# Performance work log

Measured on AMD Instinct MI355X. Metric: run time of the kernel, lower is better.

Reference implementation:

```python
import jax, jax.numpy as jnp
import numpy as np

N_NODES, E_TOT, E_ACT = 20000, 250000, 200000
LAT, OH = 128, 128
M0, M1, M2 = 64, 32, 16            # irreps_out: 64x0e + 32x1o + 16x2e
D_IR = M0 + 3 * M1 + 5 * M2        # 240
G = M1 + M2                        # gate scalars (48)
T0 = M0 + G                        # tp m=0 scalar channels (112)
I0, I1, I2 = 3 * M0, 3 * M1, 3 * M2  # tp input muls (center|edge|neighbor)


def _split(x, m0, m1, m2):
    e = x.shape[0]
    return (x[:, :m0],
            x[:, m0:m0 + 3 * m1].reshape(e, m1, 3),
            x[:, m0 + 3 * m1:].reshape(e, m2, 5))


def _merge(s0, s1, s2):
    e = s0.shape[0]
    return jnp.concatenate([s0, s1.reshape(e, -1), s2.reshape(e, -1)], axis=-1)


def _mlp(x, ws, bs):
    for i, (w, b) in enumerate(zip(ws, bs)):
        x = x @ w + b
        if i < len(ws) - 1:
            x = jax.nn.silu(x)
    return x


def _forward(latents, node_features, edge_features, cutoff_coeffs, edge_one_hot,
             wigner_D1, wigner_D2,
             W0, W1r, W1i, W2r, W2i, Gw, Gb,
             P0, P0b, P1, P2, Ew, Eb, ln_g, ln_b,
             A1, A1b, A2, A2b, A3, A3b,
             B1, B1b, B2, B2b, B3, B3b,
             O0, O1, O2,
             edge_index, active_edges):
    ec = edge_index[0][active_edges]
    en = edge_index[1][active_edges]
    # gather node features per edge (equivariant_norm_type='none' -> identity norms)
    nc0, nc1, nc2 = _split(node_features[ec], M0, M1, M2)
    ef0, ef1, ef2 = _split(edge_features, M0, M1, M2)
    nn0, nn1, nn2 = _split(node_features[en], M0, M1, M2)
    x0 = jnp.concatenate([nc0, ef0, nn0], -1)   # [E,192]
    x1 = jnp.concatenate([nc1, ef1, nn1], 1)    # [E,96,3]
    x2 = jnp.concatenate([nc2, ef2, nn2], 1)    # [E,48,5]
    lat_a = latents[active_edges]
    # --- SO(2) linear: rotate into edge frame, per-m mixing, latent gains, rotate back ---
    r1 = jnp.einsum('eij,euj->eui', wigner_D1, x1)
    r2 = jnp.einsum('eij,euj->eui', wigner_D2, x2)
    in0 = jnp.concatenate([x0, r1[:, :, 1], r2[:, :, 2]], -1)   # m=0 [E,336]
    o_m0 = in0 @ W0.T                                           # [E,160]
    ip1 = jnp.concatenate([r1[:, :, 2], r2[:, :, 3]], -1)       # m=+1 [E,144]
    im1 = jnp.concatenate([r1[:, :, 0], r2[:, :, 1]], -1)       # m=-1
    op1 = ip1 @ W1r.T - im1 @ W1i.T                             # [E,48]
    on1 = ip1 @ W1i.T + im1 @ W1r.T
    op2 = r2[:, :, 4] @ W2r.T - r2[:, :, 0] @ W2i.T             # [E,16]
    on2 = r2[:, :, 4] @ W2i.T + r2[:, :, 0] @ W2r.T
    g = lat_a @ Gw + Gb                                         # per-edge gains [E,224]
    o_m0 = o_m0 * g[:, :160]
    g1 = g[:, 160:208]; g2 = g[:, 208:224]
    op1 = op1 * g1; on1 = on1 * g1; op2 = op2 * g2; on2 = on2 * g2
    y0 = o_m0[:, :T0]
    y1 = jnp.stack([on1[:, :M1], o_m0[:, T0:T0 + M1], op1[:, :M1]], -1)          # [E,32,3]
    y2 = jnp.stack([on2, on1[:, M1:], o_m0[:, T0 + M1:], op1[:, M1:], op2], -1)  # [E,16,5]
    y1 = jnp.einsum('eji,euj->eui', wigner_D1, y1)
    y2 = jnp.einsum('eji,euj->eui', wigner_D2, y2)
    # --- gate activation ---
    gates = jax.nn.sigmoid(y0[:, M0:])
    z0 = jax.nn.silu(y0[:, :M0])
    z1 = y1 * gates[:, :M1, None]
    z2 = y2 * gates[:, M1:, None]
    # --- lin_post: per-l channel mixing, fan-in normalized, bias on scalars ---
    z0 = z0 @ P0.T / np.sqrt(M0) + P0b
    z1 = jnp.einsum('uv,evm->eum', P1, z1) / np.sqrt(M1)
    z2 = jnp.einsum('uv,evm->eum', P2, z2) / np.sqrt(M2)
    scalars = z0                                               # taken before weighting
    # --- E3ElementLinear: per-edge per-channel weights from latents ---
    w = lat_a @ Ew + Eb                                        # [E,112]
    z0 = z0 * w[:, :M0]
    z1 = z1 * w[:, M0:M0 + M1, None]
    z2 = z2 * w[:, M0 + M1:, None]
    new_edge = _merge(z0, z1, z2)
    # --- latent update: LN -> mlp1(ln_lat||scalars) -> mlp2(h||one_hot) -> cutoff ---
    mu = lat_a.mean(-1, keepdims=True)
    var = ((lat_a - mu) ** 2).mean(-1, keepdims=True)
    ln_lat = (lat_a - mu) * jax.lax.rsqrt(var + 1e-5) * ln_g + ln_b
    h = _mlp(jnp.concatenate([ln_lat, scalars], -1), (A1, A2, A3), (A1b, A2b, A3b))
    h = _mlp(jnp.concatenate([h, edge_one_hot], -1), (B1, B2, B3), (B1b, B2b, B3b))
    new_lat = cutoff_coeffs[active_edges][:, None] * h
    # --- residual update (res_update_params buffer = 0) ---
    u = jax.nn.sigmoid(jnp.asarray(0.0, new_edge.dtype))
    c_old = jax.lax.rsqrt(u * u + 1.0)
    c_new = u * c_old
    edge_out = c_old * edge_features + c_new * new_edge        # identity residual path
    latents_out = latents.at[active_edges].set(c_new * new_lat + c_old * lat_a)
    # --- layer one-hot tensor product (uvu with 128x0e) ---
    f0, f1, f2 = _split(edge_out, M0, M1, M2)
    s = 1.0 / np.sqrt(OH)
    t0 = f0 * (edge_one_hot @ O0.T) * s
    t1 = f1 * (edge_one_hot @ O1.T)[:, :, None] * s
    t2 = f2 * (edge_one_hot @ O2.T)[:, :, None] * s
    edge_out = edge_out + _merge(t0, t1, t2)
    return edge_out, latents_out


def setup_inputs() -> dict:
    key = jax.random.key(0)
    ks = iter(jax.random.split(key, 64))
    nrm = lambda sh, s=0.05: jax.random.normal(next(ks), sh, jnp.float32) * s
    inp = dict(
        latents=nrm((E_TOT, LAT), 1.0),
        node_features=nrm((N_NODES, D_IR), 1.0),
        edge_features=nrm((E_ACT, D_IR), 1.0),
        cutoff_coeffs=jax.random.uniform(next(ks), (E_TOT,), jnp.float32),
        edge_one_hot=jax.random.uniform(next(ks), (E_ACT, OH), jnp.float32),
        wigner_D1=nrm((E_ACT, 3, 3), 0.5),
        wigner_D2=nrm((E_ACT, 5, 5), 0.3),
        W0=nrm((160, I0 + I1 + I2)), W1r=nrm((48, 144)), W1i=nrm((48, 144)),
        W2r=nrm((16, 48)), W2i=nrm((16, 48)),
        Gw=nrm((LAT, 224)), Gb=jnp.ones((224,), jnp.float32),
        P0=nrm((M0, M0)), P0b=nrm((M0,)), P1=nrm((M1, M1)), P2=nrm((M2, M2)),
        Ew=nrm((LAT, M0 + M1 + M2)), Eb=jnp.ones((M0 + M1 + M2,), jnp.float32),
        ln_g=jnp.ones((LAT,), jnp.float32), ln_b=jnp.zeros((LAT,), jnp.float32),
        A1=nrm((LAT + M0, LAT)), A1b=nrm((LAT,)),
        A2=nrm((LAT, LAT)), A2b=nrm((LAT,)),
        A3=nrm((LAT, LAT)), A3b=nrm((LAT,)),
        B1=nrm((LAT + OH, LAT)), B1b=nrm((LAT,)),
        B2=nrm((LAT, LAT)), B2b=nrm((LAT,)),
        B3=nrm((LAT, LAT)), B3b=nrm((LAT,)),
        O0=nrm((M0, OH)), O1=nrm((M1, OH)), O2=nrm((M2, OH)),
        edge_index=jax.random.randint(next(ks), (2, E_TOT), 0, N_NODES, jnp.int32),
        active_edges=jnp.sort(jax.random.permutation(next(ks), E_TOT)[:E_ACT]).astype(jnp.int32),
    )
    return inp


def reference(latents, node_features, edge_features, cutoff_coeffs, edge_one_hot,
              wigner_D1, wigner_D2,
              W0, W1r, W1i, W2r, W2i, Gw, Gb,
              P0, P0b, P1, P2, Ew, Eb, ln_g, ln_b,
              A1, A1b, A2, A2b, A3, A3b,
              B1, B1b, B2, B2b, B3, B3b,
              O0, O1, O2, edge_index, active_edges):
    return _forward(latents, node_features, edge_features, cutoff_coeffs, edge_one_hot,
                    wigner_D1, wigner_D2,
                    W0, W1r, W1i, W2r, W2i, Gw, Gb,
                    P0, P0b, P1, P2, Ew, Eb, ln_g, ln_b,
                    A1, A1b, A2, A2b, A3, A3b,
                    B1, B1b, B2, B2b, B3, B3b,
                    O0, O1, O2, edge_index, active_edges)
```

## Files before the change

### kernel.cpp

```cpp
#include <hip/hip_runtime.h>

typedef unsigned short us_t;
typedef short bf16x8 __attribute__((ext_vector_type(8)));
typedef float f32x4 __attribute__((ext_vector_type(4)));

#define E_ACT 200000
#define E_TOT 250000
#define DIR   240
#define C_OLD 0.8944271909999159f
#define C_NEW 0.4472135954999579f
#define S_OH  0.08838834764831845f

#define WO_W0   0
#define WO_W1P  56320
#define WO_W1M  70144
#define WO_W2P  83968
#define WO_W2M  85504
#define WO_GW   87040
#define WO_EW   115712
#define WO_A1   130048
#define WO_A2   154624
#define WO_A3   171008
#define WO_B1   187392
#define WO_B2   220160
// ... 102 lines not shown
        a[ks] = av;
    }
}

__device__ __forceinline__ void gemmW0g(
    const us_t* __restrict__ in0s, const us_t* __restrict__ wbase,
    const bf16x8 latA[4], const float* __restrict__ Gb,
    int nt0, int nt1, us_t* __restrict__ om0g, int lane)
{
    const int r = lane & 15, g = lane >> 4;
    f32x4 w0a = {0.f,0.f,0.f,0.f}, w0b = w0a, ga = w0a, gb2 = w0a;
    const us_t* ap  = in0s + r * 360 + g * 8;
    const us_t* wp0 = wbase + WO_W0 + (size_t)(nt0 * 16 + r) * 352 + g * 8;
    const us_t* wp1 = wbase + WO_W0 + (size_t)(nt1 * 16 + r) * 352 + g * 8;
    #pragma unroll
    for (int ks = 0; ks < 11; ++ks) {
        bf16x8 a = *(const bf16x8*)(ap + ks * 32);
        w0a = MFMA(a, *(const bf16x8*)(wp0 + ks * 32), w0a);
        w0b = MFMA(a, *(const bf16x8*)(wp1 + ks * 32), w0b);
    }
    const us_t* gp0 = wbase + WO_GW + (size_t)(nt0 * 16 + r) * 128 + g * 8;
    const us_t* gp1 = wbase + WO_GW + (size_t)(nt1 * 16 + r) * 128 + g * 8;
    #pragma unroll
    for (int ks = 0; ks < 4; ++ks) {
        ga  = MFMA(latA[ks], *(const bf16x8*)(gp0 + ks * 32), ga);
        gb2 = MFMA(latA[ks], *(const bf16x8*)(gp1 + ks * 32), gb2);
    }
    float b0 = Gb[nt0 * 16 + r], b1 = Gb[nt1 * 16 + r];
    #pragma unroll
    for (int i = 0; i < 4; ++i) {
        int e = g * 4 + i;
        om0g[e * 162 + nt0 * 16 + r] = f2b(w0a[i] * (ga[i] + b0));
        om0g[e * 162 + nt1 * 16 + r] = f2b(w0b[i] * (gb2[i] + b1));
    }
}

__device__ __forceinline__ void gemmW1g(
    const us_t* __restrict__ cact1, const us_t* __restrict__ wbase,
    const bf16x8 latA[4], const float* __restrict__ Gb,
    int j, us_t* __restrict__ cp1g, us_t* __restrict__ cn1g, int lane)
{
    const int r = lane & 15, g = lane >> 4;
    f32x4 p = {0.f,0.f,0.f,0.f}, m = p, gg = p;
    const us_t* ap  = cact1 + r * 296 + g * 8;
    const us_t* wpP = wbase + WO_W1P + (size_t)(j * 16 + r) * 288 + g * 8;
    const us_t* wpM = wbase + WO_W1M + (size_t)(j * 16 + r) * 288 + g * 8;
    #pragma unroll
    for (int ks = 0; ks < 9; ++ks) {
        bf16x8 a = *(const bf16x8*)(ap + ks * 32);
        p = MFMA(a, *(const bf16x8*)(wpP + ks * 32), p);
        m = MFMA(a, *(const bf16x8*)(wpM + ks * 32), m);
    }
    const us_t* gp = wbase + WO_GW + (size_t)(160 + j * 16 + r) * 128 + g * 8;
    #pragma unroll
    for (int ks = 0; ks < 4; ++ks)
        gg = MFMA(latA[ks], *(const bf16x8*)(gp + ks * 32), gg);
    float gb = Gb[160 + j * 16 + r];
    #pragma unroll
    for (int i = 0; i < 4; ++i) {
        int e = g * 4 + i;
        float gv = gg[i] + gb;
        cp1g[e * 50 + j * 16 + r] = f2b(p[i] * gv);
        cn1g[e * 50 + j * 16 + r] = f2b(m[i] * gv);
    }
}

__device__ __forceinline__ void gemmW2g(
    const us_t* __restrict__ cact2, const us_t* __restrict__ wbase,
    const bf16x8 latA[4], const float* __restrict__ Gb,
    us_t* __restrict__ cp2g, us_t* __restrict__ cn2g, int lane)
{
    const int r = lane & 15, g = lane >> 4;
    f32x4 p = {0.f,0.f,0.f,0.f}, m = p, gg = p;
    const us_t* ap  = cact2 + r * 104 + g * 8;
    const us_t* wpP = wbase + WO_W2P + (size_t)r * 96 + g * 8;
    const us_t* wpM = wbase + WO_W2M + (size_t)r * 96 + g * 8;
    #pragma unroll
    for (int ks = 0; ks < 3; ++ks) {
        bf16x8 a = *(const bf16x8*)(ap + ks * 32);
        p = MFMA(a, *(const bf16x8*)(wpP + ks * 32), p);
        m = MFMA(a, *(const bf16x8*)(wpM + ks * 32), m);
    }
    const us_t* gp = wbase + WO_GW + (size_t)(208 + r) * 128 + g * 8;
    #pragma unroll
    for (int ks = 0; ks < 4; ++ks)
        gg = MFMA(latA[ks], *(const bf16x8*)(gp + ks * 32), gg);
    float gb = Gb[208 + r];
    #pragma unroll
    for (int i = 0; i < 4; ++i) {
        int e = g * 4 + i;
        float gv = gg[i] + gb;
        cp2g[e * 18 + r] = f2b(p[i] * gv);
        cn2g[e * 18 + r] = f2b(m[i] * gv);
    }
}

__device__ __forceinline__ void lat_gemm2(const bf16x8 a[4],
    const us_t* __restrict__ wgt, const float* __restrict__ bias,
    int nt0, int nt1, us_t* __restrict__ out, int os, int lane)
{
    const int r = lane & 15, g = lane >> 4;
    f32x4 acc0 = {0.f,0.f,0.f,0.f}, acc1 = {0.f,0.f,0.f,0.f};
    const us_t* wp0 = wgt + (size_t)(nt0 * 16 + r) * 128 + g * 8;
    const us_t* wp1 = wgt + (size_t)(nt1 * 16 + r) * 128 + g * 8;
    #pragma unroll
    for (int ks = 0; ks < 4; ++ks) {
        acc0 = MFMA(a[ks], *(const bf16x8*)(wp0 + ks * 32), acc0);
        acc1 = MFMA(a[ks], *(const bf16x8*)(wp1 + ks * 32), acc1);
    }
    float bi0 = bias[nt0 * 16 + r], bi1 = bias[nt1 * 16 + r];
    #pragma unroll
    for (int i = 0; i < 4; ++i) {
        int e = g * 4 + i;
        out[e * os + nt0 * 16 + r] = f2b(acc0[i] + bi0);
        out[e * os + nt1 * 16 + r] = f2b(acc1[i] + bi1);
    }
}

__device__ __forceinline__ void lat_gemm1(const bf16x8 a[4],
    const us_t* __restrict__ wgt, const float* __restrict__ bias,
    int nt, us_t* __restrict__ out, int os, int lane)
{
    const int r = lane & 15, g = lane >> 4;
    f32x4 acc = {0.f,0.f,0.f,0.f};
    const us_t* wp = wgt + (size_t)(nt * 16 + r) * 128 + g * 8;
    #pragma unroll
    for (int ks = 0; ks < 4; ++ks)
        acc = MFMA(a[ks], *(const bf16x8*)(wp + ks * 32), acc);
    float bi = bias[nt * 16 + r];
    #pragma unroll
    for (int i = 0; i < 4; ++i) {
        int e = g * 4 + i;
        out[e * os + nt * 16 + r] = f2b(acc[i] + bi);
    }
}

template<int KS>
__device__ __forceinline__ f32x4 pgemm(const us_t* __restrict__ actbase, int as,
                                       const us_t* __restrict__ wgt, int kp, int lane)
{
    const int r = lane & 15, g = lane >> 4;
    f32x4 acc = {0.f,0.f,0.f,0.f};
    const us_t* ap = actbase + r * as + g * 8;
    const us_t* wp = wgt + (size_t)r * kp + g * 8;
    #pragma unroll
    for (int ks = 0; ks < KS; ++ks) {
        bf16x8 a = *(const bf16x8*)(ap + ks * 32);
        bf16x8 b = *(const bf16x8*)(wp + ks * 32);
        acc = MFMA(a, b, acc);
    }
    return acc;
}

__global__ __launch_bounds__(256, 3) void k1_kernel(
    const float* __restrict__ latents,
    const float* __restrict__ node_features,
    const float* __restrict__ edge_features,
    const float* __restrict__ wD1,
    const float* __restrict__ wD2,
    const float* __restrict__ Gb,  const float* __restrict__ Eb,
    const float* __restrict__ P0b,
    const int* __restrict__ edge_index, const int* __restrict__ active_edges,
    const us_t* __restrict__ wbase,
    us_t* __restrict__ ne_ws, us_t* __restrict__ scal_ws)
{
    __shared__ __align__(16) char smem[40320];
    us_t* in0s  = (us_t*)(smem);
    us_t* cact1 = (us_t*)(smem + 11520);
    us_t* cact2 = (us_t*)(smem + 20992);
    float* D1l  = (float*)(smem + 24320);
    float* D2l  = (float*)(smem + 25088);
    int*   aes  = (int*)(smem + 26880);
    us_t* om0g  = (us_t*)(smem + 26944);
    us_t* cp1g  = (us_t*)(smem + 32128);
    us_t* cn1g  = (us_t*)(smem + 33728);
    us_t* cp2g  = (us_t*)(smem + 35328);
    us_t* cn2g  = (us_t*)(smem + 35904);
    us_t* wl    = (us_t*)(smem + 36480);
    us_t* z0l   = (us_t*)(smem);
    us_t* z1l   = (us_t*)(smem + 2304);
    us_t* z2l   = (us_t*)(smem + 5632);

    const int t  = threadIdx.x;
    const int e0 = blockIdx.x * 16;

    {
        const int e = t >> 4, l = t & 15;
        const int eg = e0 + e;
        const int ae = active_edges[eg];
        const int ec = edge_index[ae];
        const int en = edge_index[E_TOT + ae];
        if (l == 0) aes[e] = ae;

        float v1  = (l < 9) ? wD1[(size_t)eg * 9 + l] : 0.f;
        float v2a = wD2[(size_t)eg * 25 + l];
        float v2b = (l < 9) ? wD2[(size_t)eg * 25 + 16 + l] : 0.f;
        if (l < 9) D1l[e * 12 + l] = v1;
        D2l[e * 28 + l] = v2a;
        if (l < 9) D2l[e * 28 + 16 + l] = v2b;

        float d1[9], d2[25];
        #pragma unroll
        for (int i = 0; i < 9; ++i)  d1[i] = __shfl(v1, i, 16);
        #pragma unroll
        for (int i = 0; i < 16; ++i) d2[i] = __shfl(v2a, i, 16);
        #pragma unroll
        for (int i = 0; i < 9; ++i)  d2[16 + i] = __shfl(v2b, i, 16);

        const float* pc = node_features + (size_t)ec * DIR;
        const float* pe = edge_features + (size_t)eg * DIR;
        const float* pn = node_features + (size_t)en * DIR;
        us_t* in0 = in0s + e * 360;
        us_t* c1  = cact1 + e * 296;
        us_t* c2  = cact2 + e * 104;

        #pragma unroll
        for (int j = 0; j < 4; ++j) {
            int i = l + 16 * j;
            in0[i]       = f2b(pc[i]);
            in0[64 + i]  = f2b(pe[i]);
            in0[128 + i] = f2b(pn[i]);
        }
        in0[336 + l] = 0;

        #pragma unroll
        for (int jj = 0; jj < 6; ++jj) {
            int u = l + 16 * jj;
            int uu = u & 31;
            const float* sp = (u < 32 ? pc : (u < 64 ? pe : pn)) + 64 + uu * 3;
            float x0 = sp[0], x1 = sp[1], x2 = sp[2];
            float r0 = d1[0] * x0 + d1[1] * x1 + d1[2] * x2;
            float r1 = d1[3] * x0 + d1[4] * x1 + d1[5] * x2;
            float r2 = d1[6] * x0 + d1[7] * x1 + d1[8] * x2;
            c1[144 + u]  = f2b(r0);
            in0[192 + u] = f2b(r1);
            c1[u]        = f2b(r2);
        }
        #pragma unroll
        for (int jj = 0; jj < 3; ++jj) {
            int u = l + 16 * jj;
            int uu = u & 15;
            const float* sp = (u < 16 ? pc : (u < 32 ? pe : pn)) + 160 + uu * 5;
            float x0 = sp[0], x1 = sp[1], x2 = sp[2], x3 = sp[3], x4 = sp[4];
            float r[5];
            #pragma unroll
            for (int i = 0; i < 5; ++i)
                r[i] = d2[i * 5 + 0] * x0 + d2[i * 5 + 1] * x1 + d2[i * 5 + 2] * x2
                     + d2[i * 5 + 3] * x3 + d2[i * 5 + 4] * x4;
            c2[48 + u]   = f2b(r[0]);
            c1[240 + u]  = f2b(r[1]);
            in0[288 + u] = f2b(r[2]);
            c1[96 + u]   = f2b(r[3]);
            c2[u]        = f2b(r[4]);
        }
    }
    __syncthreads();

    {
        const int lane = t & 63, w = t >> 6;
        bf16x8 a[4];
        lat_fetch_a(latents, aes, lane, a);
        if (w == 0) {
            gemmW0g(in0s, wbase, a, Gb, 0, 1, om0g, lane);
            gemmW0g(in0s, wbase, a, Gb, 2, 3, om0g, lane);
        } else if (w == 1) {
            gemmW0g(in0s, wbase, a, Gb, 4, 5, om0g, lane);
            gemmW0g(in0s, wbase, a, Gb, 6, 7, om0g, lane);
        } else if (w == 2) {
            gemmW1g(cact1, wbase, a, Gb, 0, cp1g, cn1g, lane);
            gemmW1g(cact1, wbase, a, Gb, 1, cp1g, cn1g, lane);
            gemmW1g(cact1, wbase, a, Gb, 2, cp1g, cn1g, lane);
        } else {
            gemmW0g(in0s, wbase, a, Gb, 8, 9, om0g, lane);
            gemmW2g(cact2, wbase, a, Gb, cp2g, cn2g, lane);
            lat_gemm2(a, wbase + WO_EW, Eb, 0, 1, wl, 120, lane);
            lat_gemm2(a, wbase + WO_EW, Eb, 2, 3, wl, 120, lane);
            lat_gemm2(a, wbase + WO_EW, Eb, 4, 5, wl, 120, lane);
            lat_gemm1(a, wbase + WO_EW, Eb, 6, wl, 120, lane);
        }
    }
    __syncthreads();

    {
        const int e = t >> 4, l = t & 15;
        const float* D1e = D1l + e * 12;
        const float* D2e = D2l + e * 28;
        #pragma unroll
        for (int uu = 0; uu < 2; ++uu) {
            int u = l + uu * 16;
            float j0 = b2f(cn1g[e * 50 + u]);
            float j1 = b2f(om0g[e * 162 + 112 + u]);
            float j2 = b2f(cp1g[e * 50 + u]);
            float gate = sigm(b2f(om0g[e * 162 + 64 + u]));
            #pragma unroll
            for (int i = 0; i < 3; ++i) {
                float yr = D1e[0 * 3 + i] * j0 + D1e[1 * 3 + i] * j1 + D1e[2 * 3 + i] * j2;
                z1l[e * 104 + i * 32 + u] = f2b(yr * gate);
            }
        }
        {
            int u = l;
            float j0 = b2f(cn2g[e * 18 + u]);
            float j1 = b2f(cn1g[e * 50 + 32 + u]);
            float j2 = b2f(om0g[e * 162 + 144 + u]);
            float j3 = b2f(cp1g[e * 50 + 32 + u]);
            float j4 = b2f(cp2g[e * 18 + u]);
            float gate = sigm(b2f(om0g[e * 162 + 96 + u]));
            #pragma unroll
            for (int i = 0; i < 5; ++i) {
                float yr = D2e[0 * 5 + i] * j0 + D2e[1 * 5 + i] * j1 + D2e[2 * 5 + i] * j2
                         + D2e[3 * 5 + i] * j3 + D2e[4 * 5 + i] * j4;
                z2l[e * 168 + i * 32 + u] = f2b(yr * gate);
                z2l[e * 168 + i * 32 + 16 + u] = 0;
            }
        }
        #pragma unroll
        for (int ii = 0; ii < 4; ++ii) {
            int c = l + 16 * ii;
            float v = b2f(om0g[e * 162 + c]);
            z0l[e * 72 + c] = f2b(v * sigm(v));
        }
    }
    __syncthreads();

    {
        const int lane = t & 63, w = t >> 6;
        const int r = lane & 15, g = lane >> 4;
        if (w < 2) {
            #pragma unroll
            for (int jj = 0; jj < 2; ++jj) {
                int nt = 2 * w + jj;
                f32x4 acc = pgemm<2>(z0l, 72, wbase + WO_P0T + nt * 16 * 64, 64, lane);
                int n = nt * 16 + r;
                float bi = P0b[n];
                #pragma unroll
                for (int i = 0; i < 4; ++i) {
                    int e = g * 4 + i, eg = e0 + e;
                    float z0p = acc[i] * 0.125f + bi;
                    scal_ws[(size_t)eg * 64 + n] = f2b(z0p);
                    ne_ws[(size_t)eg * 240 + n] = f2b(z0p * b2f(wl[e * 120 + n]));
                }
            }
        } else if (w == 2) {
            #pragma unroll
            for (int m = 0; m < 3; ++m) {
                #pragma unroll
                for (int nt = 0; nt < 2; ++nt) {
                    f32x4 acc = pgemm<1>(z1l + m * 32, 104,
                                         wbase + WO_P1T + nt * 16 * 32, 32, lane);
                    int u = nt * 16 + r;
                    #pragma unroll
                    for (int i = 0; i < 4; ++i) {
                        int e = g * 4 + i, eg = e0 + e;
                        float wv = b2f(wl[e * 120 + 64 + u]);
                        ne_ws[(size_t)eg * 240 + 64 + u * 3 + m] =
                            f2b(acc[i] * 0.17677669529663687f * wv);
                    }
                }
            }
        } else if (w == 3) {
            #pragma unroll
            for (int m = 0; m < 5; ++m) {
                f32x4 acc = pgemm<1>(z2l + m * 32, 168, wbase + WO_P2T, 32, lane);
                int u = r;
                #pragma unroll
                for (int i = 0; i < 4; ++i) {
                    int e = g * 4 + i, eg = e0 + e;
                    float wv = b2f(wl[e * 120 + 96 + u]);
                    ne_ws[(size_t)eg * 240 + 160 + u * 5 + m] =
                        f2b(acc[i] * 0.25f * wv);
                }
            }
        }
    }
}

template<int KS, bool SILU>
__device__ __forceinline__ void mlayer(
    const us_t* __restrict__ actA, const us_t* __restrict__ actB, int split, int as,
    const us_t* __restrict__ wgt, int kp, const float* __restrict__ bias,
    us_t* __restrict__ out, int os, int lane, int w)
{
    const int r = lane & 15, g = lane >> 4;
    const int n0 = 2 * w * 16, n1 = n0 + 16;
    f32x4 a00 = {0.f,0.f,0.f,0.f}, a01 = a00, a10 = a00, a11 = a00;
    const us_t* wp0 = wgt + (size_t)(n0 + r) * kp + g * 8;
    const us_t* wp1 = wgt + (size_t)(n1 + r) * kp + g * 8;
    #pragma unroll
    for (int ks = 0; ks < KS; ++ks) {
        const us_t* ab = (ks < split) ? (actA + ks * 32) : (actB + (ks - split) * 32);
        bf16x8 f0 = *(const bf16x8*)(ab + r * as + g * 8);
        bf16x8 f1 = *(const bf16x8*)(ab + (16 + r) * as + g * 8);
        bf16x8 b0 = *(const bf16x8*)(wp0 + ks * 32);
        bf16x8 b1 = *(const bf16x8*)(wp1 + ks * 32);
        a00 = MFMA(f0, b0, a00); a01 = MFMA(f0, b1, a01);
        a10 = MFMA(f1, b0, a10); a11 = MFMA(f1, b1, a11);
    }
    float bi0 = bias[n0 + r], bi1 = bias[n1 + r];
    #pragma unroll
    for (int i = 0; i < 4; ++i) {
        int eA = g * 4 + i, eB = 16 + g * 4 + i;
        float v;
        v = a00[i] + bi0; if (SILU) v *= sigm(v); out[eA * os + n0 + r] = f2b(v);
        v = a01[i] + bi1; if (SILU) v *= sigm(v); out[eA * os + n1 + r] = f2b(v);
        v = a10[i] + bi0; if (SILU) v *= sigm(v); out[eB * os + n0 + r] = f2b(v);
        v = a11[i] + bi1; if (SILU) v *= sigm(v); out[eB * os + n1 + r] = f2b(v);
    }
}

__global__ __launch_bounds__(256) void k2_kernel(
    const float* __restrict__ latents, const float* __restrict__ cutoff,
    const float* __restrict__ one_hot,
    const float* __restrict__ ln_g, const float* __restrict__ ln_b,
    const float* __restrict__ A1b, const float* __restrict__ A2b, const float* __restrict__ A3b,
    const float* __restrict__ B1b, const float* __restrict__ B2b, const float* __restrict__ B3b,
    const int* __restrict__ active_edges,
    const us_t* __restrict__ wbase,
    const us_t* __restrict__ scal_ws, us_t* __restrict__ ohw_ws,
    float* __restrict__ out_lat)
{
    __shared__ __align__(16) char smem[39424];
    us_t* x_lds = (us_t*)(smem);
    us_t* h_a   = (us_t*)(smem + 12800);
    us_t* h_b   = (us_t*)(smem + 21504);
    us_t* ohl   = (us_t*)(smem + 30208);
    int*  aes_l = (int*)(smem + 38912);
    float* cut_l= (float*)(smem + 39040);

    const int t  = threadIdx.x;
    const int e0 = blockIdx.x * 32;
    const int lane = t & 63, w = t >> 6;

    {
        int ee = t >> 3, l8 = t & 7;
        int ae = active_edges[e0 + ee];
        if (l8 == 0) { aes_l[ee] = ae; cut_l[ee] = cutoff[ae]; }
        const float* lp = latents + (size_t)ae * 128 + l8 * 16;
        float xs[16];
        #pragma unroll
        for (int q = 0; q < 4; ++q) {
            float4 v = *(const float4*)(lp + q * 4);
            xs[q * 4 + 0] = v.x; xs[q * 4 + 1] = v.y;
            xs[q * 4 + 2] = v.z; xs[q * 4 + 3] = v.w;
        }
        float s1 = 0.f, s2 = 0.f;
        #pragma unroll
        for (int i = 0; i < 16; ++i) { s1 += xs[i]; s2 += xs[i] * xs[i]; }
        #pragma unroll
        for (int off = 1; off < 8; off <<= 1) {
            s1 += __shfl_xor(s1, off, 8);
            s2 += __shfl_xor(s2, off, 8);
        }
        float mu  = s1 * (1.f / 128.f);
        float var = s2 * (1.f / 128.f) - mu * mu;
        float rstd = rsqrtf(var + 1e-5f);
        #pragma unroll
        for (int i = 0; i < 16; ++i) {
            int li = l8 * 16 + i;
            x_lds[ee * 200 + li] = f2b((xs[i] - mu) * rstd * ln_g[li] + ln_b[li]);
        }
    }
    for (int idx = t; idx < 32 * 16; idx += 256) {
        int ee = idx >> 4, j = idx & 15;
        *(ushort4*)&x_lds[ee * 200 + 128 + j * 4] =
            *(const ushort4*)&scal_ws[(size_t)(e0 + ee) * 64 + j * 4];
    }
    for (int idx = t; idx < 32 * 32; idx += 256) {
        int ee = idx >> 5, j = idx & 31;
        float4 ov = *(const float4*)&one_hot[(size_t)(e0 + ee) * 128 + j * 4];
        ushort4 s; s.x = f2b(ov.x); s.y = f2b(ov.y); s.z = f2b(ov.z); s.w = f2b(ov.w);
        *(ushort4*)&ohl[ee * 136 + j * 4] = s;
    }
    __syncthreads();

    mlayer<6, true>(x_lds, x_lds, 6, 200, wbase + WO_A1, 192, A1b, h_a, 136, lane, w);
    __syncthreads();
    mlayer<4, true>(h_a, h_a, 4, 136, wbase + WO_A2, 128, A2b, h_b, 136, lane, w);
    __syncthreads();
    mlayer<4, false>(h_b, h_b, 4, 136, wbase + WO_A3, 128, A3b, h_a, 136, lane, w);
    __syncthreads();
    mlayer<8, true>(h_a, ohl, 4, 136, wbase + WO_B1, 256, B1b, h_b, 136, lane, w);
    __syncthreads();
    mlayer<4, true>(h_b, h_b, 4, 136, wbase + WO_B2, 128, B2b, h_a, 136, lane, w);
    __syncthreads();
    {
        const int r = lane & 15, g = lane >> 4;
        const int n0 = 2 * w * 16, n1 = n0 + 16;
        f32x4 a00 = {0.f,0.f,0.f,0.f}, a01 = a00, a10 = a00, a11 = a00;
        const us_t* wp0 = wbase + WO_B3 + (size_t)(n0 + r) * 128 + g * 8;
        const us_t* wp1 = wbase + WO_B3 + (size_t)(n1 + r) * 128 + g * 8;
        #pragma unroll
        for (int ks = 0; ks < 4; ++ks) {
            bf16x8 f0 = *(const bf16x8*)(h_a + ks * 32 + r * 136 + g * 8);
            bf16x8 f1 = *(const bf16x8*)(h_a + ks * 32 + (16 + r) * 136 + g * 8);
            bf16x8 b0 = *(const bf16x8*)(wp0 + ks * 32);
            bf16x8 b1 = *(const bf16x8*)(wp1 + ks * 32);
            a00 = MFMA(f0, b0, a00); a01 = MFMA(f0, b1, a01);
            a10 = MFMA(f1, b0, a10); a11 = MFMA(f1, b1, a11);
        }
        float bi0 = B3b[n0 + r], bi1 = B3b[n1 + r];
        #pragma unroll
        for (int i = 0; i < 4; ++i) {
            int eA = g * 4 + i, eB = 16 + g * 4 + i;
            int aeA = aes_l[eA], aeB = aes_l[eB];
            float cA = C_NEW * cut_l[eA], cB = C_NEW * cut_l[eB];
            float* oA = out_lat + (size_t)aeA * 128;
            float* oB = out_lat + (size_t)aeB * 128;
            const float* lA = latents + (size_t)aeA * 128;
            const float* lB = latents + (size_t)aeB * 128;
            oA[n0 + r] = cA * (a00[i] + bi0) + C_OLD * lA[n0 + r];
            oA[n1 + r] = cA * (a01[i] + bi1) + C_OLD * lA[n1 + r];
            oB[n0 + r] = cB * (a10[i] + bi0) + C_OLD * lB[n0 + r];
            oB[n1 + r] = cB * (a11[i] + bi1) + C_OLD * lB[n1 + r];
        }
    }

    {
        const int r = lane & 15, g = lane >> 4;
        const int cnt = (w == 3) ? 1 : 2;
        #pragma unroll
        for (int ii = 0; ii < 2; ++ii) {
            if (ii >= cnt) break;
            int nt = (ii == 0) ? w : w + 4;
            const us_t* wb2 = (nt < 4) ? (wbase + WO_O0 + (size_t)nt * 16 * 128)
                            : (nt < 6) ? (wbase + WO_O1 + (size_t)(nt - 4) * 16 * 128)
                                       : (wbase + WO_O2);
            f32x4 c0 = {0.f,0.f,0.f,0.f}, c1 = c0;
            const us_t* wp = wb2 + (size_t)r * 128 + g * 8;
            #pragma unroll
            for (int ks = 0; ks < 4; ++ks) {
                bf16x8 f0 = *(const bf16x8*)(ohl + ks * 32 + r * 136 + g * 8);
                bf16x8 f1 = *(const bf16x8*)(ohl + ks * 32 + (16 + r) * 136 + g * 8);
                bf16x8 b = *(const bf16x8*)(wp + ks * 32);
                c0 = MFMA(f0, b, c0); c1 = MFMA(f1, b, c1);
            }
            int n = nt * 16 + r;
            #pragma unroll
            for (int i = 0; i < 4; ++i) {
                int eA = e0 + g * 4 + i, eB = e0 + 16 + g * 4 + i;
                ohw_ws[(size_t)eA * 112 + n] = f2b(c0[i]);
                ohw_ws[(size_t)eB * 112 + n] = f2b(c1[i]);
            }
        }
    }
}

__global__ __launch_bounds__(256) void kfin_kernel(
    const float* __restrict__ edge_features, const us_t* __restrict__ ne_ws,
    const us_t* __restrict__ ohw_ws, float* __restrict__ out_edge)
{
    int idx = blockIdx.x * 256 + threadIdx.x;
    if (idx >= E_ACT * 60) return;
    int e = idx / 60;
    int c0 = (idx - e * 60) * 4;
    float4 ef = *(const float4*)&edge_features[(size_t)e * 240 + c0];
    ushort4 nv = *(const ushort4*)&ne_ws[(size_t)e * 240 + c0];
    float nef[4] = {b2f(nv.x), b2f(nv.y), b2f(nv.z), b2f(nv.w)};
    float eff[4] = {ef.x, ef.y, ef.z, ef.w};
    float4 ov;
    float* op = &ov.x;
    #pragma unroll
    for (int j = 0; j < 4; ++j) {
        int c = c0 + j;
        int o;
        if (c < 64)       o = c;
        else if (c < 160) o = 64 + (c - 64) / 3;
        else              o = 96 + (c - 160) / 5;
        float ohv = b2f(ohw_ws[(size_t)e * 112 + o]);
        op[j] = (C_OLD * eff[j] + C_NEW * nef[j]) * (1.f + S_OH * ohv);
    }
    *(float4*)&out_edge[(size_t)e * 240 + c0] = ov;
}

extern "C" void kernel_launch(void* const* d_in, const int* in_sizes, int n_in,
                              void* d_out, int out_size, void* d_ws, size_t ws_size,
                              hipStream_t stream)
{
    const float* latents  = (const float*)d_in[0];
    const float* node_f   = (const float*)d_in[1];
    const float* edge_f   = (const float*)d_in[2];
    const float* cutoff   = (const float*)d_in[3];
    const float* one_hot  = (const float*)d_in[4];
    const float* wD1      = (const float*)d_in[5];
    const float* wD2      = (const float*)d_in[6];
    const float* W0       = (const float*)d_in[7];
    const float* W1r      = (const float*)d_in[8];
    const float* W1i      = (const float*)d_in[9];
    const float* W2r      = (const float*)d_in[10];
    const float* W2i      = (const float*)d_in[11];
    const float* Gw       = (const float*)d_in[12];
    const float* Gb       = (const float*)d_in[13];
    const float* P0w      = (const float*)d_in[14];
    const float* P0b      = (const float*)d_in[15];
    const float* P1w      = (const float*)d_in[16];
    const float* P2w      = (const float*)d_in[17];
    const float* Ew       = (const float*)d_in[18];
    const float* Eb       = (const float*)d_in[19];
    const float* ln_g     = (const float*)d_in[20];
    const float* ln_b     = (const float*)d_in[21];
    const float* A1       = (const float*)d_in[22];
    const float* A1b      = (const float*)d_in[23];
    const float* A2       = (const float*)d_in[24];
    const float* A2b      = (const float*)d_in[25];
    const float* A3       = (const float*)d_in[26];
    const float* A3b      = (const float*)d_in[27];
    const float* B1       = (const float*)d_in[28];
    const float* B1b      = (const float*)d_in[29];
    const float* B2       = (const float*)d_in[30];
    const float* B2b      = (const float*)d_in[31];
    const float* B3       = (const float*)d_in[32];
    const float* B3b      = (const float*)d_in[33];
    const float* O0       = (const float*)d_in[34];
    const float* O1       = (const float*)d_in[35];
    const float* O2       = (const float*)d_in[36];
    const int* edge_index = (const int*)d_in[37];
    const int* act_e      = (const int*)d_in[38];

    float* out_edge = (float*)d_out;
    float* out_lat  = out_edge + (size_t)E_ACT * DIR;

    us_t* ne_ws   = (us_t*)d_ws;
    us_t* ohw_ws  = ne_ws + (size_t)E_ACT * DIR;
    us_t* scal_ws = ohw_ws + (size_t)E_ACT * 112;
    us_t* wbase   = scal_ws + (size_t)E_ACT * 64;

    prep_kernel<<<dim3((W_TOTAL + 255) / 256), dim3(256), 0, stream>>>(
        W0, W1r, W1i, W2r, W2i, Gw, Ew, A1, A2, A3, B1, B2, B3,
        O0, O1, O2, P0w, P1w, P2w, wbase);

    hipMemcpyAsync(out_lat, latents, (size_t)E_TOT * 128 * sizeof(float),
                   hipMemcpyDeviceToDevice, stream);

    k1_kernel<<<dim3(E_ACT / 16), dim3(256), 0, stream>>>(
        latents, node_f, edge_f, wD1, wD2, Gb, Eb, P0b,
        edge_index, act_e, wbase, ne_ws, scal_ws);

    k2_kernel<<<dim3(E_ACT / 32), dim3(256), 0, stream>>>(
        latents, cutoff, one_hot, ln_g, ln_b,
        A1b, A2b, A3b, B1b, B2b, B3b,
        act_e, wbase, scal_ws, ohw_ws, out_lat);

    kfin_kernel<<<dim3((E_ACT * 60 + 255) / 256), dim3(256), 0, stream>>>(
        edge_f, ne_ws, ohw_ws, out_edge);
}
```

Before: 806.6 us.

## Double block size to 512 threads and redistribute MFMA tiles across eight waves

Both fused kernels go from 256 to 512 threads per block (8 waves) and keep the same edges per block. Each phase's work is split more finely: per-edge elementwise work uses 32 lanes per edge, the W0/W1/W2/Ew GEMMs are spread over 8 waves, and the k2 MLP layers compute one 16-column tile per wave instead of two. The aim is more parallelism per block and shorter per-wave critical paths between barriers. The cost is more waves per block and some idle lanes, and launch_bounds (512,6) may force register pressure or spills.

```diff
diff --git a/kernel.cpp b/kernel.cpp
--- a/kernel.cpp
+++ b/kernel.cpp
@@ -278,7 +278,7 @@
     return acc;
 }
 
-__global__ __launch_bounds__(256, 3) void k1_kernel(
+__global__ __launch_bounds__(512, 6) void k1_kernel(
     const float* __restrict__ latents,
     const float* __restrict__ node_features,
     const float* __restrict__ edge_features,
@@ -311,27 +311,23 @@
     const int e0 = blockIdx.x * 16;
 
     {
-        const int e = t >> 4, l = t & 15;
+        const int e = t >> 5, l = t & 31;
         const int eg = e0 + e;
         const int ae = active_edges[eg];
         const int ec = edge_index[ae];
         const int en = edge_index[E_TOT + ae];
         if (l == 0) aes[e] = ae;
 
-        float v1  = (l < 9) ? wD1[(size_t)eg * 9 + l] : 0.f;
-        float v2a = wD2[(size_t)eg * 25 + l];
-        float v2b = (l < 9) ? wD2[(size_t)eg * 25 + 16 + l] : 0.f;
-        if (l < 9) D1l[e * 12 + l] = v1;
-        D2l[e * 28 + l] = v2a;
-        if (l < 9) D2l[e * 28 + 16 + l] = v2b;
+        float v1  = (l < 9)  ? wD1[(size_t)eg * 9 + l]  : 0.f;
+        float v2a = (l < 25) ? wD2[(size_t)eg * 25 + l] : 0.f;
+        if (l < 9)  D1l[e * 12 + l] = v1;
+        if (l < 25) D2l[e * 28 + l] = v2a;
 
         float d1[9], d2[25];
         #pragma unroll
-        for (int i = 0; i < 9; ++i)  d1[i] = __shfl(v1, i, 16);
-        #pragma unroll
-        for (int i = 0; i < 16; ++i) d2[i] = __shfl(v2a, i, 16);
-        #pragma unroll
-        for (int i = 0; i < 9; ++i)  d2[16 + i] = __shfl(v2b, i, 16);
+        for (int i = 0; i < 9; ++i)  d1[i] = __shfl(v1, i, 32);
+        #pragma unroll
+        for (int i = 0; i < 25; ++i) d2[i] = __shfl(v2a, i, 32);
 
         const float* pc = node_features + (size_t)ec * DIR;
         const float* pe = edge_features + (size_t)eg * DIR;
@@ -341,17 +337,17 @@
         us_t* c2  = cact2 + e * 104;
 
         #pragma unroll
-        for (int j = 0; j < 4; ++j) {
-            int i = l + 16 * j;
+        for (int j = 0; j < 2; ++j) {
+            int i = l + 32 * j;
             in0[i]       = f2b(pc[i]);
             in0[64 + i]  = f2b(pe[i]);
             in0[128 + i] = f2b(pn[i]);
         }
-        in0[336 + l] = 0;
-
-        #pragma unroll
-        for (int jj = 0; jj < 6; ++jj) {
-            int u = l + 16 * jj;
+        if (l < 16) in0[336 + l] = 0;
+
+        #pragma unroll
+        for (int jj = 0; jj < 3; ++jj) {
+            int u = l + 32 * jj;
             int uu = u & 31;
             const float* sp = (u < 32 ? pc : (u < 64 ? pe : pn)) + 64 + uu * 3;
             float x0 = sp[0], x1 = sp[1], x2 = sp[2];
@@ -363,21 +359,23 @@
             c1[u]        = f2b(r2);
         }
         #pragma unroll
-        for (int jj = 0; jj < 3; ++jj) {
-            int u = l + 16 * jj;
-            int uu = u & 15;
-            const float* sp = (u < 16 ? pc : (u < 32 ? pe : pn)) + 160 + uu * 5;
-            float x0 = sp[0], x1 = sp[1], x2 = sp[2], x3 = sp[3], x4 = sp[4];
-            float r[5];
-            #pragma unroll
-            for (int i = 0; i < 5; ++i)
-                r[i] = d2[i * 5 + 0] * x0 + d2[i * 5 + 1] * x1 + d2[i * 5 + 2] * x2
-                     + d2[i * 5 + 3] * x3 + d2[i * 5 + 4] * x4;
-            c2[48 + u]   = f2b(r[0]);
-            c1[240 + u]  = f2b(r[1]);
-            in0[288 + u] = f2b(r[2]);
-            c1[96 + u]   = f2b(r[3]);
-            c2[u]        = f2b(r[4]);
+        for (int jj = 0; jj < 2; ++jj) {
+            int u = l + 32 * jj;
+            if (u < 48) {
+                int uu = u & 15;
+                const float* sp = (u < 16 ? pc : (u < 32 ? pe : pn)) + 160 + uu * 5;
+                float x0 = sp[0], x1 = sp[1], x2 = sp[2], x3 = sp[3], x4 = sp[4];
+                float r[5];
+                #pragma unroll
+                for (int i = 0; i < 5; ++i)
+                    r[i] = d2[i * 5 + 0] * x0 + d2[i * 5 + 1] * x1 + d2[i * 5 + 2] * x2
+                         + d2[i * 5 + 3] * x3 + d2[i * 5 + 4] * x4;
+                c2[48 + u]   = f2b(r[0]);
+                c1[240 + u]  = f2b(r[1]);
+                in0[288 + u] = f2b(r[2]);
+                c1[96 + u]   = f2b(r[3]);
+                c2[u]        = f2b(r[4]);
+            }
         }
     }
     __syncthreads();
@@ -386,19 +384,15 @@
         const int lane = t & 63, w = t >> 6;
         bf16x8 a[4];
         lat_fetch_a(latents, aes, lane, a);
-        if (w == 0) {
-            gemmW0g(in0s, wbase, a, Gb, 0, 1, om0g, lane);
-            gemmW0g(in0s, wbase, a, Gb, 2, 3, om0g, lane);
-        } else if (w == 1) {
-            gemmW0g(in0s, wbase, a, Gb, 4, 5, om0g, lane);
-            gemmW0g(in0s, wbase, a, Gb, 6, 7, om0g, lane);
-        } else if (w == 2) {
+        if (w < 5) {
+            gemmW0g(in0s, wbase, a, Gb, 2 * w, 2 * w + 1, om0g, lane);
+        } else if (w == 5) {
             gemmW1g(cact1, wbase, a, Gb, 0, cp1g, cn1g, lane);
             gemmW1g(cact1, wbase, a, Gb, 1, cp1g, cn1g, lane);
+        } else if (w == 6) {
             gemmW1g(cact1, wbase, a, Gb, 2, cp1g, cn1g, lane);
+            gemmW2g(cact2, wbase, a, Gb, cp2g, cn2g, lane);
         } else {
-            gemmW0g(in0s, wbase, a, Gb, 8, 9, om0g, lane);
-            gemmW2g(cact2, wbase, a, Gb, cp2g, cn2g, lane);
             lat_gemm2(a, wbase + WO_EW, Eb, 0, 1, wl, 120, lane);
             lat_gemm2(a, wbase + WO_EW, Eb, 2, 3, wl, 120, lane);
             lat_gemm2(a, wbase + WO_EW, Eb, 4, 5, wl, 120, lane);
@@ -408,12 +402,11 @@
     __syncthreads();
 
     {
-        const int e = t >> 4, l = t & 15;
+        const int e = t >> 5, l = t & 31;
         const float* D1e = D1l + e * 12;
         const float* D2e = D2l + e * 28;
-        #pragma unroll
-        for (int uu = 0; uu < 2; ++uu) {
-            int u = l + uu * 16;
+        {
+            int u = l;
             float j0 = b2f(cn1g[e * 50 + u]);
             float j1 = b2f(om0g[e * 162 + 112 + u]);
             float j2 = b2f(cp1g[e * 50 + u]);
@@ -424,7 +417,7 @@
                 z1l[e * 104 + i * 32 + u] = f2b(yr * gate);
             }
         }
-        {
+        if (l < 16) {
             int u = l;
             float j0 = b2f(cn2g[e * 18 + u]);
             float j1 = b2f(cn1g[e * 50 + 32 + u]);
@@ -441,8 +434,8 @@
             }
         }
         #pragma unroll
-        for (int ii = 0; ii < 4; ++ii) {
-            int c = l + 16 * ii;
+        for (int ii = 0; ii < 2; ++ii) {
+            int c = l + 32 * ii;
             float v = b2f(om0g[e * 162 + c]);
             z0l[e * 72 + c] = f2b(v * sigm(v));
         }
@@ -452,49 +445,45 @@
     {
         const int lane = t & 63, w = t >> 6;
         const int r = lane & 15, g = lane >> 4;
-        if (w < 2) {
+        const float sc1 = 0.17677669529663687f;
+        if (w < 4) {
+            f32x4 acc = pgemm<2>(z0l, 72, wbase + WO_P0T + w * 16 * 64, 64, lane);
+            int n = w * 16 + r;
+            float bi = P0b[n];
             #pragma unroll
-            for (int jj = 0; jj < 2; ++jj) {
-                int nt = 2 * w + jj;
-                f32x4 acc = pgemm<2>(z0l, 72, wbase + WO_P0T + nt * 16 * 64, 64, lane);
-                int n = nt * 16 + r;
-                float bi = P0b[n];
+            for (int i = 0; i < 4; ++i) {
+                int e = g * 4 + i, eg = e0 + e;
+                float z0p = acc[i] * 0.125f + bi;
+                scal_ws[(size_t)eg * 64 + n] = f2b(z0p);
+                ne_ws[(size_t)eg * 240 + n] = f2b(z0p * b2f(wl[e * 120 + n]));
+            }
+        } else if (w == 4 || w == 5) {
+            #pragma unroll
+            for (int q = 0; q < 3; ++q) {
+                int idx = (w - 4) * 3 + q;
+                int m = idx >> 1, nt = idx & 1;
+                f32x4 acc = pgemm<1>(z1l + m * 32, 104,
+                                     wbase + WO_P1T + nt * 16 * 32, 32, lane);
+                int u = nt * 16 + r;
                 #pragma unroll
                 for (int i = 0; i < 4; ++i) {
                     int e = g * 4 + i, eg = e0 + e;
-                    float z0p = acc[i] * 0.125f + bi;
-                    scal_ws[(size_t)eg * 64 + n] = f2b(z0p);
-                    ne_ws[(size_t)eg * 240 + n] = f2b(z0p * b2f(wl[e * 120 + n]));
+                    float wv = b2f(wl[e * 120 + 64 + u]);
+                    ne_ws[(size_t)eg * 240 + 64 + u * 3 + m] = f2b(acc[i] * sc1 * wv);
                 }
             }
-        } else if (w == 2) {
-            #pragma unroll
-            for (int m = 0; m < 3; ++m) {
-                #pragma unroll
-                for (int nt = 0; nt < 2; ++nt) {
-                    f32x4 acc = pgemm<1>(z1l + m * 32, 104,
-                                         wbase + WO_P1T + nt * 16 * 32, 32, lane);
-                    int u = nt * 16 + r;
-                    #pragma unroll
-                    for (int i = 0; i < 4; ++i) {
-                        int e = g * 4 + i, eg = e0 + e;
-                        float wv = b2f(wl[e * 120 + 64 + u]);
-                        ne_ws[(size_t)eg * 240 + 64 + u * 3 + m] =
-                            f2b(acc[i] * 0.17677669529663687f * wv);
-                    }
-                }
-            }
-        } else if (w == 3) {
-            #pragma unroll
-            for (int m = 0; m < 5; ++m) {
+        } else {
+            const int mstart = (w == 6) ? 0 : 3;
+            const int mcnt   = (w == 6) ? 3 : 2;
+            for (int q = 0; q < mcnt; ++q) {
+                int m = mstart + q;
                 f32x4 acc = pgemm<1>(z2l + m * 32, 168, wbase + WO_P2T, 32, lane);
                 int u = r;
                 #pragma unroll
                 for (int i = 0; i < 4; ++i) {
                     int e = g * 4 + i, eg = e0 + e;
                     float wv = b2f(wl[e * 120 + 96 + u]);
-                    ne_ws[(size_t)eg * 240 + 160 + u * 5 + m] =
-                        f2b(acc[i] * 0.25f * wv);
+                    ne_ws[(size_t)eg * 240 + 160 + u * 5 + m] = f2b(acc[i] * 0.25f * wv);
                 }
             }
         }
@@ -502,39 +491,35 @@
 }
 
 template<int KS, bool SILU>
-__device__ __forceinline__ void mlayer(
+__device__ __forceinline__ void mlayer8(
     const us_t* __restrict__ actA, const us_t* __restrict__ actB, int split, int as,
     const us_t* __restrict__ wgt, int kp, const float* __restrict__ bias,
     us_t* __restrict__ out, int os, int lane, int w)
 {
     const int r = lane & 15, g = lane >> 4;
-    const int n0 = 2 * w * 16, n1 = n0 + 16;
-    f32x4 a00 = {0.f,0.f,0.f,0.f}, a01 = a00, a10 = a00, a11 = a00;
-    const us_t* wp0 = wgt + (size_t)(n0 + r) * kp + g * 8;
-    const us_t* wp1 = wgt + (size_t)(n1 + r) * kp + g * 8;
+    const int n0 = w * 16;
+    f32x4 a0 = {0.f,0.f,0.f,0.f}, a1 = a0;
+    const us_t* wp = wgt + (size_t)(n0 + r) * kp + g * 8;
     #pragma unroll
     for (int ks = 0; ks < KS; ++ks) {
         const us_t* ab = (ks < split) ? (actA + ks * 32) : (actB + (ks - split) * 32);
         bf16x8 f0 = *(const bf16x8*)(ab + r * as + g * 8);
         bf16x8 f1 = *(const bf16x8*)(ab + (16 + r) * as + g * 8);
-        bf16x8 b0 = *(const bf16x8*)(wp0 + ks * 32);
-        bf16x8 b1 = *(const bf16x8*)(wp1 + ks * 32);
-        a00 = MFMA(f0, b0, a00); a01 = MFMA(f0, b1, a01);
-        a10 = MFMA(f1, b0, a10); a11 = MFMA(f1, b1, a11);
-    }
-    float bi0 = bias[n0 + r], bi1 = bias[n1 + r];
+        bf16x8 b = *(const bf16x8*)(wp + ks * 32);
+        a0 = MFMA(f0, b, a0);
+        a1 = MFMA(f1, b, a1);
+    }
+    float bi = bias[n0 + r];
     #pragma unroll
     for (int i = 0; i < 4; ++i) {
         int eA = g * 4 + i, eB = 16 + g * 4 + i;
         float v;
-        v = a00[i] + bi0; if (SILU) v *= sigm(v); out[eA * os + n0 + r] = f2b(v);
-        v = a01[i] + bi1; if (SILU) v *= sigm(v); out[eA * os + n1 + r] = f2b(v);
-        v = a10[i] + bi0; if (SILU) v *= sigm(v); out[eB * os + n0 + r] = f2b(v);
-        v = a11[i] + bi1; if (SILU) v *= sigm(v); out[eB * os + n1 + r] = f2b(v);
-    }
-}
-
-__global__ __launch_bounds__(256) void k2_kernel(
+        v = a0[i] + bi; if (SILU) v *= sigm(v); out[eA * os + n0 + r] = f2b(v);
+        v = a1[i] + bi; if (SILU) v *= sigm(v); out[eB * os + n0 + r] = f2b(v);
+    }
+}
+
+__global__ __launch_bounds__(512, 6) void k2_kernel(
     const float* __restrict__ latents, const float* __restrict__ cutoff,
     const float* __restrict__ one_hot,
     const float* __restrict__ ln_g, const float* __restrict__ ln_b,
@@ -558,40 +543,36 @@
     const int lane = t & 63, w = t >> 6;
 
     {
-        int ee = t >> 3, l8 = t & 7;
+        int ee = t >> 4, l16 = t & 15;
         int ae = active_edges[e0 + ee];
-        if (l8 == 0) { aes_l[ee] = ae; cut_l[ee] = cutoff[ae]; }
-        const float* lp = latents + (size_t)ae * 128 + l8 * 16;
-        float xs[16];
-        #pragma unroll
-        for (int q = 0; q < 4; ++q) {
-            float4 v = *(const float4*)(lp + q * 4);
-            xs[q * 4 + 0] = v.x; xs[q * 4 + 1] = v.y;
-            xs[q * 4 + 2] = v.z; xs[q * 4 + 3] = v.w;
-        }
+        if (l16 == 0) { aes_l[ee] = ae; cut_l[ee] = cutoff[ae]; }
+        const float* lp = latents + (size_t)ae * 128 + l16 * 8;
+        float4 va = *(const float4*)lp;
+        float4 vb = *(const float4*)(lp + 4);
+        float xs[8] = {va.x, va.y, va.z, va.w, vb.x, vb.y, vb.z, vb.w};
         float s1 = 0.f, s2 = 0.f;
         #pragma unroll
-        for (int i = 0; i < 16; ++i) { s1 += xs[i]; s2 += xs[i] * xs[i]; }
-        #pragma unroll
-        for (int off = 1; off < 8; off <<= 1) {
-            s1 += __shfl_xor(s1, off, 8);
-            s2 += __shfl_xor(s2, off, 8);
+        for (int i = 0; i < 8; ++i) { s1 += xs[i]; s2 += xs[i] * xs[i]; }
+        #pragma unroll
+        for (int off = 1; off < 16; off <<= 1) {
+            s1 += __shfl_xor(s1, off, 16);
+            s2 += __shfl_xor(s2, off, 16);
         }
         float mu  = s1 * (1.f / 128.f);
         float var = s2 * (1.f / 128.f) - mu * mu;
         float rstd = rsqrtf(var + 1e-5f);
         #pragma unroll
-        for (int i = 0; i < 16; ++i) {
-            int li = l8 * 16 + i;
+        for (int i = 0; i < 8; ++i) {
+            int li = l16 * 8 + i;
             x_lds[ee * 200 + li] = f2b((xs[i] - mu) * rstd * ln_g[li] + ln_b[li]);
         }
     }
-    for (int idx = t; idx < 32 * 16; idx += 256) {
+    for (int idx = t; idx < 32 * 16; idx += 512) {
         int ee = idx >> 4, j = idx & 15;
         *(ushort4*)&x_lds[ee * 200 + 128 + j * 4] =
             *(const ushort4*)&scal_ws[(size_t)(e0 + ee) * 64 + j * 4];
     }
-    for (int idx = t; idx < 32 * 32; idx += 256) {
+    for (int idx = t; idx < 32 * 32; idx += 512) {
         int ee = idx >> 5, j = idx & 31;
         float4 ov = *(const float4*)&one_hot[(size_t)(e0 + ee) * 128 + j * 4];
         ushort4 s; s.x = f2b(ov.x); s.y = f2b(ov.y); s.z = f2b(ov.z); s.w = f2b(ov.w);
@@ -599,74 +580,63 @@
     }
     __syncthreads();
 
-    mlayer<6, true>(x_lds, x_lds, 6, 200, wbase + WO_A1, 192, A1b, h_a, 136, lane, w);
-    __syncthreads();
-    mlayer<4, true>(h_a, h_a, 4, 136, wbase + WO_A2, 128, A2b, h_b, 136, lane, w);
-    __syncthreads();
-    mlayer<4, false>(h_b, h_b, 4, 136, wbase + WO_A3, 128, A3b, h_a, 136, lane, w);
-    __syncthreads();
-    mlayer<8, true>(h_a, ohl, 4, 136, wbase + WO_B1, 256, B1b, h_b, 136, lane, w);
-    __syncthreads();
-    mlayer<4, true>(h_b, h_b, 4, 136, wbase + WO_B2, 128, B2b, h_a, 136, lane, w);
+    mlayer8<6, true>(x_lds, x_lds, 6, 200, wbase + WO_A1, 192, A1b, h_a, 136, lane, w);
+    __syncthreads();
+    mlayer8<4, true>(h_a, h_a, 4, 136, wbase + WO_A2, 128, A2b, h_b, 136, lane, w);
+    __syncthreads();
+    mlayer8<4, false>(h_b, h_b, 4, 136, wbase + WO_A3, 128, A3b, h_a, 136, lane, w);
+    __syncthreads();
+    mlayer8<8, true>(h_a, ohl, 4, 136, wbase + WO_B1, 256, B1b, h_b, 136, lane, w);
+    __syncthreads();
+    mlayer8<4, true>(h_b, h_b, 4, 136, wbase + WO_B2, 128, B2b, h_a, 136, lane, w);
     __syncthreads();
     {
         const int r = lane & 15, g = lane >> 4;
-        const int n0 = 2 * w * 16, n1 = n0 + 16;
-        f32x4 a00 = {0.f,0.f,0.f,0.f}, a01 = a00, a10 = a00, a11 = a00;
-        const us_t* wp0 = wbase + WO_B3 + (size_t)(n0 + r) * 128 + g * 8;
-        const us_t* wp1 = wbase + WO_B3 + (size_t)(n1 + r) * 128 + g * 8;
+        const int n0 = w * 16;
+        f32x4 a0 = {0.f,0.f,0.f,0.f}, a1 = a0;
+        const us_t* wp = wbase + WO_B3 + (size_t)(n0 + r) * 128 + g * 8;
         #pragma unroll
         for (int ks = 0; ks < 4; ++ks) {
             bf16x8 f0 = *(const bf16x8*)(h_a + ks * 32 + r * 136 + g * 8);
             bf16x8 f1 = *(const bf16x8*)(h_a + ks * 32 + (16 + r) * 136 + g * 8);
-            bf16x8 b0 = *(const bf16x8*)(wp0 + ks * 32);
-            bf16x8 b1 = *(const bf16x8*)(wp1 + ks * 32);
-            a00 = MFMA(f0, b0, a00); a01 = MFMA(f0, b1, a01);
-            a10 = MFMA(f1, b0, a10); a11 = MFMA(f1, b1, a11);
-        }
-        float bi0 = B3b[n0 + r], bi1 = B3b[n1 + r];
+            bf16x8 b = *(const bf16x8*)(wp + ks * 32);
+            a0 = MFMA(f0, b, a0);
+            a1 = MFMA(f1, b, a1);
+        }
+        float bi = B3b[n0 + r];
         #pragma unroll
         for (int i = 0; i < 4; ++i) {
             int eA = g * 4 + i, eB = 16 + g * 4 + i;
             int aeA = aes_l[eA], aeB = aes_l[eB];
             float cA = C_NEW * cut_l[eA], cB = C_NEW * cut_l[eB];
-            float* oA = out_lat + (size_t)aeA * 128;
-            float* oB = out_lat + (size_t)aeB * 128;
-            const float* lA = latents + (size_t)aeA * 128;
-            const float* lB = latents + (size_t)aeB * 128;
-            oA[n0 + r] = cA * (a00[i] + bi0) + C_OLD * lA[n0 + r];
-            oA[n1 + r] = cA * (a01[i] + bi1) + C_OLD * lA[n1 + r];
-            oB[n0 + r] = cB * (a10[i] + bi0) + C_OLD * lB[n0 + r];
-            oB[n1 + r] = cB * (a11[i] + bi1) + C_OLD * lB[n1 + r];
-        }
-    }
-
-    {
+            out_lat[(size_t)aeA * 128 + n0 + r] =
+                cA * (a0[i] + bi) + C_OLD * latents[(size_t)aeA * 128 + n0 + r];
+            out_lat[(size_t)aeB * 128 + n0 + r] =
+                cB * (a1[i] + bi) + C_OLD * latents[(size_t)aeB * 128 + n0 + r];
+        }
+    }
+
+    if (w < 7) {
         const int r = lane & 15, g = lane >> 4;
-        const int cnt = (w == 3) ? 1 : 2;
-        #pragma unroll
-        for (int ii = 0; ii < 2; ++ii) {
-            if (ii >= cnt) break;
-            int nt = (ii == 0) ? w : w + 4;
-            const us_t* wb2 = (nt < 4) ? (wbase + WO_O0 + (size_t)nt * 16 * 128)
-                            : (nt < 6) ? (wbase + WO_O1 + (size_t)(nt - 4) * 16 * 128)
-                                       : (wbase + WO_O2);
-            f32x4 c0 = {0.f,0.f,0.f,0.f}, c1 = c0;
-            const us_t* wp = wb2 + (size_t)r * 128 + g * 8;
-            #pragma unroll
-            for (int ks = 0; ks < 4; ++ks) {
-                bf16x8 f0 = *(const bf16x8*)(ohl + ks * 32 + r * 136 + g * 8);
-                bf16x8 f1 = *(const bf16x8*)(ohl + ks * 32 + (16 + r) * 136 + g * 8);
-                bf16x8 b = *(const bf16x8*)(wp + ks * 32);
-                c0 = MFMA(f0, b, c0); c1 = MFMA(f1, b, c1);
-            }
-            int n = nt * 16 + r;
-            #pragma unroll
-            for (int i = 0; i < 4; ++i) {
-                int eA = e0 + g * 4 + i, eB = e0 + 16 + g * 4 + i;
-                ohw_ws[(size_t)eA * 112 + n] = f2b(c0[i]);
-                ohw_ws[(size_t)eB * 112 + n] = f2b(c1[i]);
-            }
+        const int nt = w;
+        const us_t* wb2 = (nt < 4) ? (wbase + WO_O0 + (size_t)nt * 16 * 128)
+                        : (nt < 6) ? (wbase + WO_O1 + (size_t)(nt - 4) * 16 * 128)
+                                   : (wbase + WO_O2);
+        f32x4 c0 = {0.f,0.f,0.f,0.f}, c1 = c0;
+        const us_t* wp = wb2 + (size_t)r * 128 + g * 8;
+        #pragma unroll
+        for (int ks = 0; ks < 4; ++ks) {
+            bf16x8 f0 = *(const bf16x8*)(ohl + ks * 32 + r * 136 + g * 8);
+            bf16x8 f1 = *(const bf16x8*)(ohl + ks * 32 + (16 + r) * 136 + g * 8);
+            bf16x8 b = *(const bf16x8*)(wp + ks * 32);
+            c0 = MFMA(f0, b, c0); c1 = MFMA(f1, b, c1);
+        }
+        int n = nt * 16 + r;
+        #pragma unroll
+        for (int i = 0; i < 4; ++i) {
+            int eA = e0 + g * 4 + i, eB = e0 + 16 + g * 4 + i;
+            ohw_ws[(size_t)eA * 112 + n] = f2b(c0[i]);
+            ohw_ws[(size_t)eB * 112 + n] = f2b(c1[i]);
         }
     }
 }
@@ -757,11 +727,11 @@
     hipMemcpyAsync(out_lat, latents, (size_t)E_TOT * 128 * sizeof(float),
                    hipMemcpyDeviceToDevice, stream);
 
-    k1_kernel<<<dim3(E_ACT / 16), dim3(256), 0, stream>>>(
+    k1_kernel<<<dim3(E_ACT / 16), dim3(512), 0, stream>>>(
         latents, node_f, edge_f, wD1, wD2, Gb, Eb, P0b,
         edge_index, act_e, wbase, ne_ws, scal_ws);
 
-    k2_kernel<<<dim3(E_ACT / 32), dim3(256), 0, stream>>>(
+    k2_kernel<<<dim3(E_ACT / 32), dim3(512), 0, stream>>>(
         latents, cutoff, one_hot, ln_g, ln_b,
         A1b, A2b, A3b, B1b, B2b, B3b,
         act_e, wbase, scal_ws, ohw_ws, out_lat);
```

Result: slower. 870.7 us (+7.9%).
